# Optimization experiments

Measured on AMD Instinct MI355X. Metric: run time of the kernel, lower is better.

## Reference

```python
import jax, jax.numpy as jnp
import numpy as np

NUM_ENT_CLASS = 150
NORMED_REL_VEC_DIST = False


def box_cxcywh_to_xyxy(b):
    cx, cy, w, h = b[..., 0], b[..., 1], b[..., 2], b[..., 3]
    return jnp.stack([cx - 0.5 * w, cy - 0.5 * h, cx + 0.5 * w, cy + 0.5 * h], axis=-1)


def box_xyxy_to_cxcywh(b):
    x0, y0, x1, y1 = b[..., 0], b[..., 1], b[..., 2], b[..., 3]
    return jnp.stack([(x0 + x1) * 0.5, (y0 + y1) * 0.5, x1 - x0, y1 - y0], axis=-1)


def generalized_box_iou(a, b):
    # a: [N,4], b: [M,4], xyxy -> [N,M]
    area_a = (a[:, 2] - a[:, 0]) * (a[:, 3] - a[:, 1])
    area_b = (b[:, 2] - b[:, 0]) * (b[:, 3] - b[:, 1])
    lt = jnp.maximum(a[:, None, :2], b[None, :, :2])
    rb = jnp.minimum(a[:, None, 2:], b[None, :, 2:])
    wh = jnp.clip(rb - lt, 0.0)
    inter = wh[..., 0] * wh[..., 1]
    union = area_a[:, None] + area_b[None, :] - inter
    iou = inter / union
    lt_c = jnp.minimum(a[:, None, :2], b[None, :, :2])
    rb_c = jnp.maximum(a[:, None, 2:], b[None, :, 2:])
    wh_c = jnp.clip(rb_c - lt_c, 0.0)
    area_c = wh_c[..., 0] * wh_c[..., 1]
    return iou - (area_c - union) / area_c


def cdist_l2(a, b):
    # a: [N,C], b: [M,C] -> [N,M] euclidean distance (gram-matrix form)
    d2 = (jnp.sum(a * a, -1)[:, None] + jnp.sum(b * b, -1)[None, :]
          - 2.0 * (a @ b.T))
    return jnp.sqrt(jnp.maximum(d2, 1e-12))


def _per_image(ent_box_n, ent_logits, ro_logits, rs_logits, ro_box_n, rs_box_n,
               rel_vec_n, scale):
    # scale: [4] = [w, h, w, h]
    ent_box = box_cxcywh_to_xyxy(ent_box_n) * scale[None, :]           # [Ne,4] pixels
    ent_cnter = box_xyxy_to_cxcywh(ent_box)[..., :2]                    # [Ne,2]
    ent_cnter_normed = ent_box_n[..., :2]

    # num_ent_class (150) != logits dim (151) -> softmax, drop background
    ro_dist = jax.nn.softmax(ro_logits, axis=-1)[..., :-1]              # [Nr,150]
    rs_dist = jax.nn.softmax(rs_logits, axis=-1)[..., :-1]
    ent_prob = jax.nn.softmax(ent_logits, axis=-1)[..., :-1]            # [Ne,150]
    ent_score = jnp.max(ent_prob, axis=-1)                              # [Ne]

    ro_box = box_cxcywh_to_xyxy(ro_box_n) * scale[None, :]              # [Nr,4]
    rs_box = box_cxcywh_to_xyxy(rs_box_n) * scale[None, :]
    rel_vec = rel_vec_n * scale[None, :]                                # [Nr,4]

    if NORMED_REL_VEC_DIST:
        vec, sc, oc = rel_vec_n, ent_cnter_normed, ent_cnter_normed
    else:
        vec, sc, oc = rel_vec, ent_cnter, ent_cnter

    # L1 distance of rel-vector endpoints to entity centers -> [Nr,Ne]
    dist_s = (jnp.abs(vec[:, None, 0] - sc[None, :, 0])
              + jnp.abs(vec[:, None, 1] - sc[None, :, 1]))
    dist_o = (jnp.abs(vec[:, None, 2] - oc[None, :, 0])
              + jnp.abs(vec[:, None, 3] - oc[None, :, 1]))
    match_vec_sub = 1.0 / (dist_s + 1.0)
    match_vec_obj = 1.0 / (dist_o + 1.0)

    m_s = ent_score[None, :] * match_vec_sub                            # conf-weighted
    m_o = ent_score[None, :] * match_vec_obj

    sub_giou = jnp.clip(generalized_box_iou(ent_box, rs_box), 0.0)      # [Ne,Nr]
    obj_giou = jnp.clip(generalized_box_iou(ent_box, ro_box), 0.0)

    sub_cls = 1.0 / (cdist_l2(rs_dist, ent_prob) + 1.0)                 # [Nr,Ne]
    obj_cls = 1.0 / (cdist_l2(ro_dist, ent_prob) + 1.0)

    dist_s_final = m_s * sub_cls * sub_giou.T                           # [Nr,Ne]
    dist_o_final = m_o * obj_cls * obj_giou.T
    return dist_s_final, dist_o_final


def setup_inputs() -> dict:
    key = jax.random.key(0)
    ks = jax.random.split(key, 8)
    B, Ne, Nr, C1 = 64, 500, 500, NUM_ENT_CLASS + 1
    inp = {
        "pred_boxes": jax.random.uniform(ks[0], (B, Ne, 4), jnp.float32),
        "pred_logits": jax.random.normal(ks[1], (B, Ne, C1), jnp.float32),
        "pred_rel_obj_logits": jax.random.normal(ks[2], (B, Nr, C1), jnp.float32),
        "pred_rel_sub_logits": jax.random.normal(ks[3], (B, Nr, C1), jnp.float32),
        "pred_rel_obj_box": jax.random.uniform(ks[4], (B, Nr, 4), jnp.float32),
        "pred_rel_sub_box": jax.random.uniform(ks[5], (B, Nr, 4), jnp.float32),
        "pred_rel_vec": jax.random.uniform(ks[6], (B, Nr, 4), jnp.float32),
        "target_sizes": 600.0 + 600.0 * jax.random.uniform(ks[7], (B, 2), jnp.float32),
    }
    return inp


def reference(pred_boxes, pred_logits, pred_rel_obj_logits, pred_rel_sub_logits,
              pred_rel_obj_box, pred_rel_sub_box, pred_rel_vec, target_sizes):
    img_h, img_w = target_sizes[:, 0], target_sizes[:, 1]
    scale_fct = jnp.stack([img_w, img_h, img_w, img_h], axis=1)  # [B,4]
    sub_dist, obj_dist = jax.vmap(_per_image)(
        pred_boxes, pred_logits, pred_rel_obj_logits, pred_rel_sub_logits,
        pred_rel_obj_box, pred_rel_sub_box, pred_rel_vec, scale_fct)
    return sub_dist, obj_dist
```

## Files before the change

### kernel.cpp

```cpp
#include <hip/hip_runtime.h>
#include <math.h>

#define NB   64
#define NPT  500
#define C1   151
#define CM1  150
#define EAF  12
#define RAF  20

#define GRP_ELEMS  2560
#define IMG_ELEMS  (32 * GRP_ELEMS)
#define PROB_ELEMS ((size_t)NB * IMG_ELEMS)

typedef __bf16 bf16x8 __attribute__((ext_vector_type(8)));
typedef float  f32x4  __attribute__((ext_vector_type(4)));

__device__ __forceinline__ float rcpf(float x) { return __builtin_amdgcn_rcpf(x); }
__device__ __forceinline__ float rsqf(float x) { return __builtin_amdgcn_rsqf(x); }

extern "C" __global__ void __launch_bounds__(256)
k_pre(const float* __restrict__ boxes, const float* __restrict__ ent_logits,
      const float* __restrict__ ro_logits, const float* __restrict__ rs_logits,
      const float* __restrict__ ro_box, const float* __restrict__ rs_box,
      const float* __restrict__ rel_vec, const float* __restrict__ tsz,
      __bf16* __restrict__ entP, __bf16* __restrict__ rsP, __bf16* __restrict__ roP,
      float* __restrict__ entAux, float* __restrict__ relAux)
{
    const int tid = threadIdx.x;
    const int q   = tid & 15;
    const int rl  = tid >> 4;
    const int bx  = blockIdx.x;
    const int set = bx / 2000;
    const int rowIdx = (bx - set * 2000) * 16 + rl;
    const int b = rowIdx / 500;
    const int i = rowIdx - b * 500;

    const float* src = (set == 0 ? ent_logits : (set == 1 ? rs_logits : ro_logits))
                       + (size_t)rowIdx * C1;

    float x[10];
    #pragma unroll
    for (int t = 0; t < 9; ++t) x[t] = src[q + 16 * t];
    x[9] = (q <= 6) ? src[q + 144] : -INFINITY;

    float mAll = x[0];
    #pragma unroll
    for (int t = 1; t < 10; ++t) mAll = fmaxf(mAll, x[t]);
    float mKept = x[0];
    #pragma unroll
    for (int t = 1; t < 9; ++t) mKept = fmaxf(mKept, x[t]);
    if (q <= 5) mKept = fmaxf(mKept, x[9]);

    #pragma unroll
    for (int off = 1; off < 16; off <<= 1) {
        mAll  = fmaxf(mAll,  __shfl_xor(mAll,  off, 16));
        mKept = fmaxf(mKept, __shfl_xor(mKept, off, 16));
    }

    float e[10], s = 0.f, s2 = 0.f;
    #pragma unroll
    for (int t = 0; t < 9; ++t) {
        e[t] = __expf(x[t] - mAll);
        s  += e[t];
        s2 += e[t] * e[t];
    }
    e[9] = (q <= 6) ? __expf(x[9] - mAll) : 0.f;
    s += e[9];
    if (q <= 5) s2 += e[9] * e[9];

    #pragma unroll
    for (int off = 1; off < 16; off <<= 1) {
        s  += __shfl_xor(s,  off, 16);
        s2 += __shfl_xor(s2, off, 16);
    }

    const float inv = rcpf(s);
    const float pm  = __expf(mKept - mAll) * inv;
    const float nn  = s2 * inv * inv;

    __bf16* dstT = (set == 0 ? entP : (set == 1 ? rsP : roP));
    const int g  = i >> 4, ir = i & 15;
    __bf16* dst = dstT + ((size_t)b * 32 + g) * GRP_ELEMS + ir * 8 + (q & 7);
    const int qh = q >> 3;
    #pragma unroll
    for (int t = 0; t < 9; ++t)
        dst[(2 * t + qh) * 128] = (__bf16)(e[t] * inv);
    dst[(18 + qh) * 128] = (q <= 5) ? (__bf16)(e[9] * inv) : (__bf16)0.f;

    if (q == 0) {
        const float hh = tsz[b * 2 + 0];
        const float ww = tsz[b * 2 + 1];
        if (set == 0) {
            const float* bb = boxes + (size_t)rowIdx * 4;
            const float cx = bb[0], cy = bb[1], bw = bb[2], bh = bb[3];
            const float X0 = (cx - 0.5f * bw) * ww, Y0 = (cy - 0.5f * bh) * hh;
            const float X1 = (cx + 0.5f * bw) * ww, Y1 = (cy + 0.5f * bh) * hh;
            float* A = entAux + (size_t)rowIdx * EAF;
            A[0] = pm;
            A[1] = 0.5f * (X0 + X1);
            A[2] = 0.5f * (Y0 + Y1);
            A[3] = nn;
            A[4] = X0; A[5] = Y0; A[6] = X1; A[7] = Y1;
            A[8] = (X1 - X0) * (Y1 - Y0);
        } else if (set == 1) {
            const float* bb = rs_box  + (size_t)rowIdx * 4;
            const float* vv = rel_vec + (size_t)rowIdx * 4;
            const float cx = bb[0], cy = bb[1], bw = bb[2], bh = bb[3];
            float* A = relAux + (size_t)rowIdx * RAF;
            const float X0 = (cx - 0.5f * bw) * ww, Y0 = (cy - 0.5f * bh) * hh;
            const float X1 = (cx + 0.5f * bw) * ww, Y1 = (cy + 0.5f * bh) * hh;
            A[0] = X0; A[1] = Y0; A[2] = X1; A[3] = Y1;
            A[8]  = vv[0] * ww; A[9]  = vv[1] * hh;
            A[10] = vv[2] * ww; A[11] = vv[3] * hh;
            A[12] = nn;
            A[14] = (X1 - X0) * (Y1 - Y0);
        } else {
            const float* bb = ro_box + (size_t)rowIdx * 4;
            const float cx = bb[0], cy = bb[1], bw = bb[2], bh = bb[3];
            float* A = relAux + (size_t)rowIdx * RAF;
            const float X0 = (cx - 0.5f * bw) * ww, Y0 = (cy - 0.5f * bh) * hh;
            const float X1 = (cx + 0.5f * bw) * ww, Y1 = (cy + 0.5f * bh) * hh;
            A[4] = X0; A[5] = Y0; A[6] = X1; A[7] = Y1;
            A[13] = nn;
            A[15] = (X1 - X0) * (Y1 - Y0);
        }
    }
}

template <bool FULL>
__device__ __forceinline__ void epilogue(
    const float (*eA)[EAF], const float (*rA)[RAF],
    const f32x4* accS, const f32x4* accO,
    int lr, int kq, int wv, int b, int e0T, int r0T,
    float* __restrict__ outS, float* __restrict__ outO)
{
    f32x4 ev0[4], ev1[4];
    float eArea[4];
    #pragma unroll
    for (int et = 0; et < 4; ++et) {
        const float* ep = eA[et * 16 + lr];
        ev0[et] = *(const f32x4*)(ep);
        ev1[et] = *(const f32x4*)(ep + 4);
        eArea[et] = ep[8];
    }

    const unsigned baseR0 = ((unsigned)b * NPT + (unsigned)(r0T + wv * 16 + kq * 4)) * NPT;
    const unsigned eBase  = (unsigned)(e0T + lr);

    #pragma unroll
    for (int reg = 0; reg < 4; ++reg) {
        const int rIdx = wv * 16 + kq * 4 + reg;
        const bool rOK = FULL || (r0T + rIdx < NPT);
        const float* rp = rA[rIdx];
        const f32x4 rsB = *(const f32x4*)(rp);
        const f32x4 roB = *(const f32x4*)(rp + 4);
        const f32x4 vv  = *(const f32x4*)(rp + 8);
        const f32x4 rn  = *(const f32x4*)(rp + 12);
        const unsigned rowOff = baseR0 + (unsigned)reg * NPT;

        #pragma unroll
        for (int et = 0; et < 4; ++et) {
            const float score = ev0[et][0], ecx = ev0[et][1], ecy = ev0[et][2], en2 = ev0[et][3];
            const float ex0 = ev1[et][0], ey0 = ev1[et][1], ex1 = ev1[et][2], ey1 = ev1[et][3];
            const float aE = eArea[et];

            const float iwS = fmaxf(fminf(ex1, rsB[2]) - fmaxf(ex0, rsB[0]), 0.f);
            const float ihS = fmaxf(fminf(ey1, rsB[3]) - fmaxf(ey0, rsB[1]), 0.f);
            const float inS = iwS * ihS;
            const float unS = aE + rn[2] - inS;
            const float aCS = (fmaxf(ex1, rsB[2]) - fminf(ex0, rsB[0]))
                            * (fmaxf(ey1, rsB[3]) - fminf(ey0, rsB[1]));
            const float gS  = fmaxf(fmaf(fmaf(inS, aCS, unS * unS), rcpf(unS * aCS), -1.f), 0.f);

            const float iwO = fmaxf(fminf(ex1, roB[2]) - fmaxf(ex0, roB[0]), 0.f);
            const float ihO = fmaxf(fminf(ey1, roB[3]) - fmaxf(ey0, roB[1]), 0.f);
            const float inO = iwO * ihO;
            const float unO = aE + rn[3] - inO;
            const float aCO = (fmaxf(ex1, roB[2]) - fminf(ex0, roB[0]))
                            * (fmaxf(ey1, roB[3]) - fminf(ey0, roB[1]));
            const float gO  = fmaxf(fmaf(fmaf(inO, aCO, unO * unO), rcpf(unO * aCO), -1.f), 0.f);

            const float d2s = fmaxf(fmaf(-2.f, accS[et][reg], rn[0] + en2), 1e-12f);
            const float d2o = fmaxf(fmaf(-2.f, accO[et][reg], rn[1] + en2), 1e-12f);
            const float dS  = d2s * rsqf(d2s);
            const float dO  = d2o * rsqf(d2o);
            const float distS = fabsf(vv[0] - ecx) + fabsf(vv[1] - ecy);
            const float distO = fabsf(vv[2] - ecx) + fabsf(vv[3] - ecy);
            const float qS = rcpf((distS + 1.f) * (dS + 1.f));
            const float qO = rcpf((distO + 1.f) * (dO + 1.f));

            const float vS = score * qS * gS;
            const float vO = score * qO * gO;

            const unsigned o = rowOff + eBase + (unsigned)(et * 16);
            if (FULL || (rOK && (int)(eBase + et * 16) < NPT)) {
                outS[o] = vS;
                outO[o] = vO;
            }
        }
    }
}

extern "C" __global__ void __launch_bounds__(256, 4)
k_main(const __bf16* __restrict__ entP, const __bf16* __restrict__ rsP,
       const __bf16* __restrict__ roP, const float* __restrict__ eAuxG,
       const float* __restrict__ rAuxG,
       float* __restrict__ outS, float* __restrict__ outO)
{
    __shared__ __align__(16) __bf16 sEnt[4 * GRP_ELEMS];
    __shared__ __align__(16) float eA[64][EAF];
    __shared__ __align__(16) float rA[64][RAF];

    const int tid = threadIdx.x;
    const int b   = blockIdx.x;
    const int e0T = (blockIdx.y & 7) * 64;
    const int r0T = (blockIdx.y >> 3) * 64;

    const int wv   = tid >> 6;
    const int lane = tid & 63;
    const int lr   = lane & 15;
    const int kq   = lane >> 4;

    const int gR = (r0T >> 4) + wv;
    const int gE = (e0T >> 4);
    const __bf16* rsBase = rsP  + ((size_t)b * 32 + gR) * GRP_ELEMS + lr * 8;
    const __bf16* roBase = roP  + ((size_t)b * 32 + gR) * GRP_ELEMS + lr * 8;
    const __bf16* entSrc = entP + ((size_t)b * 32 + gE) * GRP_ELEMS;

    bf16x8 ars[5], aro[5];
    #pragma unroll
    for (int ks = 0; ks < 5; ++ks) {
        const int kOff = (ks * 4 + kq) * 128;
        ars[ks] = *(const bf16x8*)(rsBase + kOff);
        aro[ks] = *(const bf16x8*)(roBase + kOff);
    }

    #pragma unroll
    for (int it = 0; it < 5; ++it) {
        const int off = it * 4096 + wv * 1024;
        __builtin_amdgcn_global_load_lds(
            (const __attribute__((address_space(1))) unsigned int*)
                ((const char*)entSrc + off + lane * 16),
            (__attribute__((address_space(3))) unsigned int*)
                ((char*)sEnt + off),
            16, 0, 0);
    }

    {
        const float4 z = {0.f, 0.f, 0.f, 0.f};
        for (int t = tid; t < 64 * (EAF / 4); t += 256) {
            const int e = t / (EAF / 4), qq = t % (EAF / 4);
            const int ge = e0T + e;
            ((float4*)eA[e])[qq] = (ge < NPT)
                ? ((const float4*)(eAuxG + ((size_t)b * NPT + ge) * EAF))[qq] : z;
        }
        for (int t = tid; t < 64 * (RAF / 4); t += 256) {
            const int r = t / (RAF / 4), qq = t % (RAF / 4);
            const int gr = r0T + r;
            ((float4*)rA[r])[qq] = (gr < NPT)
                ? ((const float4*)(rAuxG + ((size_t)b * NPT + gr) * RAF))[qq] : z;
        }
    }
    __syncthreads();

    f32x4 accS[4] = {{0,0,0,0},{0,0,0,0},{0,0,0,0},{0,0,0,0}};
    f32x4 accO[4] = {{0,0,0,0},{0,0,0,0},{0,0,0,0},{0,0,0,0}};

    #pragma unroll
    for (int ks = 0; ks < 5; ++ks) {
        const int kOff = (ks * 4 + kq) * 128 + lr * 8;
        #pragma unroll
        for (int et = 0; et < 4; ++et) {
            const bf16x8 be = *(const bf16x8*)&sEnt[et * GRP_ELEMS + kOff];
            accS[et] = __builtin_amdgcn_mfma_f32_16x16x32_bf16(ars[ks], be, accS[et], 0, 0, 0);
            accO[et] = __builtin_amdgcn_mfma_f32_16x16x32_bf16(aro[ks], be, accO[et], 0, 0, 0);
        }
    }

    if (e0T + 64 <= NPT && r0T + 64 <= NPT) {
        epilogue<true >(eA, rA, accS, accO, lr, kq, wv, b, e0T, r0T, outS, outO);
    } else {
        epilogue<false>(eA, rA, accS, accO, lr, kq, wv, b, e0T, r0T, outS, outO);
    }
}

extern "C" void kernel_launch(void* const* d_in, const int* in_sizes, int n_in,
                              void* d_out, int out_size, void* d_ws, size_t ws_size,
                              hipStream_t stream)
{
    const float* boxes      = (const float*)d_in[0];
    const float* ent_logits = (const float*)d_in[1];
    const float* ro_logits  = (const float*)d_in[2];
    const float* rs_logits  = (const float*)d_in[3];
    const float* ro_box     = (const float*)d_in[4];
    const float* rs_box     = (const float*)d_in[5];
    const float* rel_vec    = (const float*)d_in[6];
    const float* tsz        = (const float*)d_in[7];

    __bf16* entP = (__bf16*)d_ws;
    __bf16* rsP  = entP + PROB_ELEMS;
    __bf16* roP  = rsP  + PROB_ELEMS;
    float*  eAux = (float*)(roP + PROB_ELEMS);
    float*  rAux = eAux + (size_t)NB * NPT * EAF;

    float* outS = (float*)d_out;
    float* outO = outS + (size_t)NB * NPT * NPT;

    hipLaunchKernelGGL(k_pre, dim3(6000), dim3(256), 0, stream,
                       boxes, ent_logits, ro_logits, rs_logits,
                       ro_box, rs_box, rel_vec, tsz,
                       entP, rsP, roP, eAux, rAux);

    hipLaunchKernelGGL(k_main, dim3(64, 64), dim3(256), 0, stream,
                       entP, rsP, roP, eAux, rAux, outS, outO);
}
```

Before: 234.3 us.

## Stage pre-kernel probabilities in LDS and fold GIoU divisions into one reciprocal

The pre-kernel now maps each block to one 16-row group per image. It writes the softmax tiles into shared memory and then copies them to global memory with coalesced 16-byte stores. It also zero-fills the padding rows, so the grid becomes 6144 blocks. In the main epilogue, the enclosing-box area now comes from precomputed widths and heights via an identity (sum of widths minus signed overlap), and the two reciprocals per pair are merged into one. This reduces ALU and transcendental work in the output-bound epilogue, at the cost of a slightly different floating-point ordering and extra aux fields.

```diff
diff --git a/kernel.cpp b/kernel.cpp
--- a/kernel.cpp
+++ b/kernel.cpp
@@ -26,22 +26,33 @@
       __bf16* __restrict__ entP, __bf16* __restrict__ rsP, __bf16* __restrict__ roP,
       float* __restrict__ entAux, float* __restrict__ relAux)
 {
+    __shared__ __align__(16) __bf16 sP[GRP_ELEMS];
+
     const int tid = threadIdx.x;
     const int q   = tid & 15;
     const int rl  = tid >> 4;
     const int bx  = blockIdx.x;
-    const int set = bx / 2000;
-    const int rowIdx = (bx - set * 2000) * 16 + rl;
-    const int b = rowIdx / 500;
-    const int i = rowIdx - b * 500;
+    const int set = bx >> 11;
+    const int rem = bx & 2047;
+    const int b   = rem >> 5;
+    const int g   = rem & 31;
+    const int i   = g * 16 + rl;
+    const bool valid = (i < NPT);
+    const int rowIdx = b * NPT + i;
 
     const float* src = (set == 0 ? ent_logits : (set == 1 ? rs_logits : ro_logits))
                        + (size_t)rowIdx * C1;
 
     float x[10];
-    #pragma unroll
-    for (int t = 0; t < 9; ++t) x[t] = src[q + 16 * t];
-    x[9] = (q <= 6) ? src[q + 144] : -INFINITY;
+    if (valid) {
+        #pragma unroll
+        for (int t = 0; t < 9; ++t) x[t] = src[q + 16 * t];
+        x[9] = (q <= 6) ? src[q + 144] : -INFINITY;
+    } else {
+        #pragma unroll
+        for (int t = 0; t < 9; ++t) x[t] = 0.f;
+        x[9] = -INFINITY;
+    }
 
     float mAll = x[0];
     #pragma unroll
@@ -78,16 +89,14 @@
     const float pm  = __expf(mKept - mAll) * inv;
     const float nn  = s2 * inv * inv;
 
-    __bf16* dstT = (set == 0 ? entP : (set == 1 ? rsP : roP));
-    const int g  = i >> 4, ir = i & 15;
-    __bf16* dst = dstT + ((size_t)b * 32 + g) * GRP_ELEMS + ir * 8 + (q & 7);
-    const int qh = q >> 3;
+    const int base = rl * 8 + (q & 7);
+    const int qh   = q >> 3;
     #pragma unroll
     for (int t = 0; t < 9; ++t)
-        dst[(2 * t + qh) * 128] = (__bf16)(e[t] * inv);
-    dst[(18 + qh) * 128] = (q <= 5) ? (__bf16)(e[9] * inv) : (__bf16)0.f;
-
-    if (q == 0) {
+        sP[(2 * t + qh) * 128 + base] = valid ? (__bf16)(e[t] * inv) : (__bf16)0.f;
+    sP[(18 + qh) * 128 + base] = (valid && q <= 5) ? (__bf16)(e[9] * inv) : (__bf16)0.f;
+
+    if (q == 0 && valid) {
         const float hh = tsz[b * 2 + 0];
         const float ww = tsz[b * 2 + 1];
         if (set == 0) {
@@ -102,6 +111,8 @@
             A[3] = nn;
             A[4] = X0; A[5] = Y0; A[6] = X1; A[7] = Y1;
             A[8] = (X1 - X0) * (Y1 - Y0);
+            A[9] = X1 - X0;
+            A[10] = Y1 - Y0;
         } else if (set == 1) {
             const float* bb = rs_box  + (size_t)rowIdx * 4;
             const float* vv = rel_vec + (size_t)rowIdx * 4;
@@ -114,6 +125,8 @@
             A[10] = vv[2] * ww; A[11] = vv[3] * hh;
             A[12] = nn;
             A[14] = (X1 - X0) * (Y1 - Y0);
+            A[16] = X1 - X0;
+            A[17] = Y1 - Y0;
         } else {
             const float* bb = ro_box + (size_t)rowIdx * 4;
             const float cx = bb[0], cy = bb[1], bw = bb[2], bh = bb[3];
@@ -123,8 +136,18 @@
             A[4] = X0; A[5] = Y0; A[6] = X1; A[7] = Y1;
             A[13] = nn;
             A[15] = (X1 - X0) * (Y1 - Y0);
-        }
-    }
+            A[18] = X1 - X0;
+            A[19] = Y1 - Y0;
+        }
+    }
+
+    __syncthreads();
+
+    __bf16* dstT = (set == 0 ? entP : (set == 1 ? rsP : roP));
+    float4* dstG = (float4*)(dstT + ((size_t)b * 32 + g) * GRP_ELEMS);
+    const float4* srcL = (const float4*)sP;
+    dstG[tid] = srcL[tid];
+    if (tid < 64) dstG[256 + tid] = srcL[256 + tid];
 }
 
 template <bool FULL>
@@ -135,13 +158,13 @@
     float* __restrict__ outS, float* __restrict__ outO)
 {
     f32x4 ev0[4], ev1[4];
-    float eArea[4];
+    float eAr[4], eW[4], eH[4];
     #pragma unroll
     for (int et = 0; et < 4; ++et) {
         const float* ep = eA[et * 16 + lr];
         ev0[et] = *(const f32x4*)(ep);
         ev1[et] = *(const f32x4*)(ep + 4);
-        eArea[et] = ep[8];
+        eAr[et] = ep[8]; eW[et] = ep[9]; eH[et] = ep[10];
     }
 
     const unsigned baseR0 = ((unsigned)b * NPT + (unsigned)(r0T + wv * 16 + kq * 4)) * NPT;
@@ -156,41 +179,38 @@
         const f32x4 roB = *(const f32x4*)(rp + 4);
         const f32x4 vv  = *(const f32x4*)(rp + 8);
         const f32x4 rn  = *(const f32x4*)(rp + 12);
+        const f32x4 rw  = *(const f32x4*)(rp + 16);
         const unsigned rowOff = baseR0 + (unsigned)reg * NPT;
 
         #pragma unroll
         for (int et = 0; et < 4; ++et) {
             const float score = ev0[et][0], ecx = ev0[et][1], ecy = ev0[et][2], en2 = ev0[et][3];
             const float ex0 = ev1[et][0], ey0 = ev1[et][1], ex1 = ev1[et][2], ey1 = ev1[et][3];
-            const float aE = eArea[et];
-
-            const float iwS = fmaxf(fminf(ex1, rsB[2]) - fmaxf(ex0, rsB[0]), 0.f);
-            const float ihS = fmaxf(fminf(ey1, rsB[3]) - fmaxf(ey0, rsB[1]), 0.f);
-            const float inS = iwS * ihS;
-            const float unS = aE + rn[2] - inS;
-            const float aCS = (fmaxf(ex1, rsB[2]) - fminf(ex0, rsB[0]))
-                            * (fmaxf(ey1, rsB[3]) - fminf(ey0, rsB[1]));
-            const float gS  = fmaxf(fmaf(fmaf(inS, aCS, unS * unS), rcpf(unS * aCS), -1.f), 0.f);
-
-            const float iwO = fmaxf(fminf(ex1, roB[2]) - fmaxf(ex0, roB[0]), 0.f);
-            const float ihO = fmaxf(fminf(ey1, roB[3]) - fmaxf(ey0, roB[1]), 0.f);
-            const float inO = iwO * ihO;
-            const float unO = aE + rn[3] - inO;
-            const float aCO = (fmaxf(ex1, roB[2]) - fminf(ex0, roB[0]))
-                            * (fmaxf(ey1, roB[3]) - fminf(ey0, roB[1]));
-            const float gO  = fmaxf(fmaf(fmaf(inO, aCO, unO * unO), rcpf(unO * aCO), -1.f), 0.f);
-
-            const float d2s = fmaxf(fmaf(-2.f, accS[et][reg], rn[0] + en2), 1e-12f);
-            const float d2o = fmaxf(fmaf(-2.f, accO[et][reg], rn[1] + en2), 1e-12f);
-            const float dS  = d2s * rsqf(d2s);
-            const float dO  = d2o * rsqf(d2o);
-            const float distS = fabsf(vv[0] - ecx) + fabsf(vv[1] - ecy);
-            const float distO = fabsf(vv[2] - ecx) + fabsf(vv[3] - ecy);
-            const float qS = rcpf((distS + 1.f) * (dS + 1.f));
-            const float qO = rcpf((distO + 1.f) * (dO + 1.f));
-
-            const float vS = score * qS * gS;
-            const float vO = score * qO * gO;
+            const float aE = eAr[et];
+
+            const float iwrS = fminf(ex1, rsB[2]) - fmaxf(ex0, rsB[0]);
+            const float ihrS = fminf(ey1, rsB[3]) - fmaxf(ey0, rsB[1]);
+            const float inS  = fmaxf(iwrS, 0.f) * fmaxf(ihrS, 0.f);
+            const float aCS  = ((eW[et] + rw[0]) - iwrS) * ((eH[et] + rw[1]) - ihrS);
+            const float unS  = (aE + rn[2]) - inS;
+            const float uaS  = unS * aCS;
+            const float numS = fmaxf(score * (fmaf(inS, aCS, unS * unS) - uaS), 0.f);
+            const float d2s  = fmaxf(fmaf(-2.f, accS[et][reg], rn[0] + en2), 1e-12f);
+            const float dS   = d2s * rsqf(d2s);
+            const float distS= fabsf(vv[0] - ecx) + fabsf(vv[1] - ecy);
+            const float vS   = numS * rcpf(uaS * (distS + 1.f) * (dS + 1.f));
+
+            const float iwrO = fminf(ex1, roB[2]) - fmaxf(ex0, roB[0]);
+            const float ihrO = fminf(ey1, roB[3]) - fmaxf(ey0, roB[1]);
+            const float inO  = fmaxf(iwrO, 0.f) * fmaxf(ihrO, 0.f);
+            const float aCO  = ((eW[et] + rw[2]) - iwrO) * ((eH[et] + rw[3]) - ihrO);
+            const float unO  = (aE + rn[3]) - inO;
+            const float uaO  = unO * aCO;
+            const float numO = fmaxf(score * (fmaf(inO, aCO, unO * unO) - uaO), 0.f);
+            const float d2o  = fmaxf(fmaf(-2.f, accO[et][reg], rn[1] + en2), 1e-12f);
+            const float dO   = d2o * rsqf(d2o);
+            const float distO= fabsf(vv[2] - ecx) + fabsf(vv[3] - ecy);
+            const float vO   = numO * rcpf(uaO * (distO + 1.f) * (dO + 1.f));
 
             const unsigned o = rowOff + eBase + (unsigned)(et * 16);
             if (FULL || (rOK && (int)(eBase + et * 16) < NPT)) {
@@ -306,7 +326,7 @@
     float* outS = (float*)d_out;
     float* outO = outS + (size_t)NB * NPT * NPT;
 
-    hipLaunchKernelGGL(k_pre, dim3(6000), dim3(256), 0, stream,
+    hipLaunchKernelGGL(k_pre, dim3(6144), dim3(256), 0, stream,
                        boxes, ent_logits, ro_logits, rs_logits,
                        ro_box, rs_box, rel_vec, tsz,
                        entP, rsP, roP, eAux, rAux);
```

Result: no change. 231.1 us (-1.4%).
